# Kernel optimization log

Measured on AMD Instinct MI355X. Metric: run time of the kernel, lower is better.

The kernel has to match this reference:

```python
import jax, jax.numpy as jnp
import numpy as np

B, C, W, H = 32, 512, 28, 28  # input spatial = 2*init_width x 2*init_height
HEADS = 8


def setup_inputs() -> dict:
    key = jax.random.key(0)
    ks = jax.random.split(key, 9)
    d = C // HEADS
    s = 0.05
    return {
        "x": jax.random.normal(ks[0], (B, C, W, H), jnp.float32),
        # 1x1 conv weights == dense [out_c, in_c] + bias
        "wq": jax.random.normal(ks[1], (C, C), jnp.float32) * s,
        "bq": jax.random.normal(ks[2], (C,), jnp.float32) * s,
        "wk": jax.random.normal(ks[3], (C, C), jnp.float32) * s,
        "bk": jax.random.normal(ks[4], (C,), jnp.float32) * s,
        "wv": jax.random.normal(ks[5], (C, C), jnp.float32) * s,
        "bv": jax.random.normal(ks[6], (C,), jnp.float32) * s,
        "rel_h": jax.random.normal(ks[7], (1, HEADS, d, 1, H), jnp.float32),
        "rel_w": jax.random.normal(ks[8], (1, HEADS, d, W, 1), jnp.float32),
    }


def reference(x, wq, bq, wk, bk, wv, bv, rel_h, rel_w):
    b, c, w, h = x.shape
    heads = rel_h.shape[1]
    d = c // heads
    n = w * h

    def proj(wt, bi):
        # 1x1 conv == per-pixel dense over channels
        y = jnp.einsum('oc,bcwh->bowh', wt, x) + bi[None, :, None, None]
        return y.reshape(b, heads, d, n)  # [B, H, d, N]

    q = proj(wq, bq)
    k = proj(wk, bk)
    v = proj(wv, bv)

    # content-content: q^T k -> [B, H, N, N]
    cc = jnp.einsum('bhdn,bhdm->bhnm', q, k)
    # relative position bias: (rel_h + rel_w) broadcast to [H, d, 2w0*2h0] = [H, d, N]
    pos = (rel_h + rel_w).reshape(heads, d, n)
    # content-position: pos^T @ q -> [B, H, N, N]
    cp = jnp.einsum('hdp,bhdn->bhpn', pos, q)

    attn = jax.nn.softmax(cc + cp, axis=-1)  # softmax over last dim
    # out = v @ attn^T : [B, H, d, N]
    out = jnp.einsum('bhdn,bhmn->bhdm', v, attn)
    return out.reshape(b, c, w, h)
```

## Files before the change

### kernel.cpp

```cpp
#include <hip/hip_runtime.h>


#define BATCH 32
#define CCH   512
#define NHEAD 8
#define DH    64
#define NTOK  784
#define WSP   28
#define OT    128
#define NT    112
#define WLD   40
#define CH    64
#define NCHUNK 13
#define NIBLK  7
#define KQLD  136
#define VLD   72

typedef unsigned short u16;
typedef unsigned int   u32;
typedef short  short8  __attribute__((ext_vector_type(8)));
typedef float  floatx4 __attribute__((ext_vector_type(4)));

__device__ __forceinline__ u16 f2bf(float f) {
    union { float f; u32 i; } v; v.f = f;
    u32 x = v.i;
    return (u16)((x + 0x7FFFu + ((x >> 16) & 1u)) >> 16);
}
__device__ __forceinline__ u32 f2u(float f) { union { float f; u32 i; } v; v.f = f; return v.i; }
__device__ __forceinline__ float u2f(u32 u) { union { u32 i; float f; } v; v.i = u; return v.f; }

__device__ __forceinline__ u32 packsplit(float f) {
    const u32 hib = f2u(f) & 0xFFFF0000u;
    const float lo = f - u2f(hib);
    return ((u32)f2bf(lo) << 16) | (hib >> 16);
}

__global__ __launch_bounds__(256)
void pack_weights(const float* __restrict__ wq, const float* __restrict__ wk,
                  const float* __restrict__ wv,
                  u32* __restrict__ Wqp, u32* __restrict__ Wkp, u32* __restrict__ Wvp)
{
    const int i = blockIdx.x * 256 + threadIdx.x;
    if (i < CCH * CCH) {
        Wqp[i] = packsplit(wq[i]);
        Wkp[i] = packsplit(wk[i]);
        Wvp[i] = packsplit(wv[i]);
    }
}

__global__ __launch_bounds__(256)
void pack_x(const float* __restrict__ x, u32* __restrict__ Xp, int b0, size_t count)
{
    const size_t i = (size_t)blockIdx.x * 256 + threadIdx.x;
    if (i < count)
        Xp[i] = packsplit(x[(size_t)b0 * CCH * NTOK + i]);
}

__global__ __launch_bounds__(512)
void qkv_proj(const u32* __restrict__ Xp,
              const u32* __restrict__ Wqp, const float* __restrict__ bq,
              const u32* __restrict__ Wkp, const float* __restrict__ bk,
              const u32* __restrict__ Wvp, const float* __restrict__ bv,
              u32* __restrict__ Qp, u32* __restrict__ Kp, u16* __restrict__ Vo,
              int nbatch)
{
    const int t    = threadIdx.x;
    const int lane = t & 63;
    const int wid  = t >> 6;
    const int z    = blockIdx.z;
    const int proj = z / nbatch;
    const int bl   = z - proj * nbatch;
    const int o0   = blockIdx.y * OT;
    const int n0   = blockIdx.x * NT;

    const u32*   Wp   = (proj == 0) ? Wqp : (proj == 1) ? Wkp : Wvp;
    const float* bias = (proj == 0) ? bq  : (proj == 1) ? bk  : bv;

    __shared__ u16 wh[OT][WLD], wl[OT][WLD];
    __shared__ u16 xh[NT][WLD], xl[NT][WLD];

    const int m    = lane & 15;
    const int quad = lane >> 4;

    floatx4 acc[7];
    #pragma unroll
    for (int j = 0; j < 7; j++) acc[j] = (floatx4){0.f, 0.f, 0.f, 0.f};

    const int wo = t >> 2;
    const int wc = (t & 3) * 8;
    const int xc = t >> 3;
    const int xn = (t & 7) * 14;

    const size_t xbase = (size_t)bl * CCH * NTOK;

    for (int c0 = 0; c0 < CCH; c0 += 32) {
        uint4 wv0 = *reinterpret_cast<const uint4*>(&Wp[(size_t)(o0 + wo) * CCH + c0 + wc]);
        uint4 wv1 = *reinterpret_cast<const uint4*>(&Wp[(size_t)(o0 + wo) * CCH + c0 + wc + 4]);
        u32 xreg[14];
        if (t < 256) {
            #pragma unroll
            for (int u = 0; u < 7; u++) {
                const uint2 p = *reinterpret_cast<const uint2*>(&Xp[xbase + (size_t)(c0 + xc) * NTOK + n0 + xn + 2 * u]);
                xreg[2 * u] = p.x; xreg[2 * u + 1] = p.y;
            }
        }
        __syncthreads();
        {
            const u32 wr[8] = {wv0.x, wv0.y, wv0.z, wv0.w, wv1.x, wv1.y, wv1.z, wv1.w};
            ushort4 h0 = make_ushort4((u16)(wr[0] & 0xFFFF), (u16)(wr[1] & 0xFFFF), (u16)(wr[2] & 0xFFFF), (u16)(wr[3] & 0xFFFF));
            ushort4 h1 = make_ushort4((u16)(wr[4] & 0xFFFF), (u16)(wr[5] & 0xFFFF), (u16)(wr[6] & 0xFFFF), (u16)(wr[7] & 0xFFFF));
            ushort4 l0 = make_ushort4((u16)(wr[0] >> 16), (u16)(wr[1] >> 16), (u16)(wr[2] >> 16), (u16)(wr[3] >> 16));
            ushort4 l1 = make_ushort4((u16)(wr[4] >> 16), (u16)(wr[5] >> 16), (u16)(wr[6] >> 16), (u16)(wr[7] >> 16));
            *reinterpret_cast<ushort4*>(&wh[wo][wc])     = h0;
            *reinterpret_cast<ushort4*>(&wh[wo][wc + 4]) = h1;
            *reinterpret_cast<ushort4*>(&wl[wo][wc])     = l0;
            *reinterpret_cast<ushort4*>(&wl[wo][wc + 4]) = l1;
        }
        if (t < 256) {
            #pragma unroll
            for (int u = 0; u < 14; u++) {
                xh[xn + u][xc] = (u16)(xreg[u] & 0xFFFFu);
                xl[xn + u][xc] = (u16)(xreg[u] >> 16);
            }
        }
        __syncthreads();

        const short8 Ah = *reinterpret_cast<const short8*>(&wh[wid * 16 + m][quad * 8]);
        const short8 Al = *reinterpret_cast<const short8*>(&wl[wid * 16 + m][quad * 8]);
        #pragma unroll
        for (int jt = 0; jt < 7; jt++) {
            const short8 Bh = *reinterpret_cast<const short8*>(&xh[jt * 16 + m][quad * 8]);
            const short8 Bl = *reinterpret_cast<const short8*>(&xl[jt * 16 + m][quad * 8]);
            acc[jt] = __builtin_amdgcn_mfma_f32_16x16x32_bf16(Ah, Bh, acc[jt], 0, 0, 0);
            acc[jt] = __builtin_amdgcn_mfma_f32_16x16x32_bf16(Ah, Bl, acc[jt], 0, 0, 0);
            acc[jt] = __builtin_amdgcn_mfma_f32_16x16x32_bf16(Al, Bh, acc[jt], 0, 0, 0);
        }
    }

    const size_t obase = (size_t)bl * CCH * NTOK;
    #pragma unroll
    for (int r = 0; r < 4; r++) {
        const int o = o0 + wid * 16 + quad * 4 + r;
        const float bi = bias[o];
        #pragma unroll
        for (int jt = 0; jt < 7; jt++) {
            const int n = n0 + jt * 16 + m;
            const float val = acc[jt][r] + bi;
            const size_t idx = obase + (size_t)o * NTOK + n;
            if (proj == 0)      Qp[idx] = packsplit(val);
            else if (proj == 1) Kp[idx] = packsplit(val);
            else                Vo[idx] = f2bf(val);
        }
    }
}

__global__ __launch_bounds__(512)
void attn_kernel(const u32* __restrict__ Qp, const u32* __restrict__ Kp,
                 const u16* __restrict__ V,
                 const float* __restrict__ rel_h, const float* __restrict__ rel_w,
                 float* __restrict__ out, int b0)
{
    const int t    = threadIdx.x;
    const int lane = t & 63;
    const int wid  = t >> 6;
    const int m    = lane & 15;
    const int quad = lane >> 4;
    const int bl   = blockIdx.x;
    const int h    = blockIdx.y;
    int i0 = blockIdx.z * 128;
    if (i0 > NTOK - 128) i0 = NTOK - 128;
    const int b  = b0 + bl;
    const int hd = h * DH;
    const size_t base  = ((size_t)bl * CCH + hd) * NTOK;
    const size_t baseo = ((size_t)b  * CCH + hd) * NTOK;

    __shared__ u16 kqh[CH][KQLD];
    __shared__ u16 kql[CH][KQLD];
    __shared__ u16 vt[DH][VLD];
    __shared__ u16 pt[128][VLD];

    short8 Bh[4], Bl[4];
    {
        const int ig = i0 + wid * 16 + m;
        const int iw = ig / WSP, ih = ig % WSP;
        #pragma unroll
        for (int c = 0; c < 4; c++) {
            union { short8 v; u16 u[8]; } hb, lb;
            #pragma unroll
            for (int idx = 0; idx < 8; idx++) {
                const int k = c * 32 + quad * 8 + idx;
                if (k < DH) {
                    const u32 p = Qp[base + (size_t)k * NTOK + ig];
                    hb.u[idx] = (u16)(p & 0xFFFFu);
                    lb.u[idx] = (u16)(p >> 16);
                } else {
                    const int d = k - DH;
                    const float pos = rel_h[(size_t)(hd + d) * WSP + ih]
                                    + rel_w[(size_t)(hd + d) * WSP + iw];
                    const u32 hib = f2u(pos) & 0xFFFF0000u;
                    hb.u[idx] = (u16)(hib >> 16);
                    lb.u[idx] = f2bf(pos - u2f(hib));
                }
            }
            Bh[c] = hb.v; Bl[c] = lb.v;
        }
    }

    floatx4 Oacc[4];
    #pragma unroll
    for (int dt = 0; dt < 4; dt++) Oacc[dt] = (floatx4){0.f, 0.f, 0.f, 0.f};
    float mrun = -1e30f, lrun = 0.f;

    const int cg4 = (t & 31) * 4;
    const int jb4 = (t >> 5) * 4;
    const int vd  = t >> 3;
    const int vj  = (t & 7) * 8;

    for (int chn = 0; chn < NCHUNK; chn++) {
        const int j0 = chn * CH;
        __syncthreads();

        {
            u32 kv[4][4];
            #pragma unroll
            for (int cc = 0; cc < 4; cc++) {
                const int c = cg4 + cc;
                const u32* src = (c < DH) ? (Kp + base + (size_t)c * NTOK)
                                          : (Qp + base + (size_t)(c - DH) * NTOK);
                const uint4 a = *reinterpret_cast<const uint4*>(&src[j0 + jb4]);
                kv[cc][0] = a.x; kv[cc][1] = a.y; kv[cc][2] = a.z; kv[cc][3] = a.w;
            }
            #pragma unroll
            for (int jj = 0; jj < 4; jj++) {
                const ushort4 hi = make_ushort4((u16)(kv[0][jj] & 0xFFFFu), (u16)(kv[1][jj] & 0xFFFFu),
                                                (u16)(kv[2][jj] & 0xFFFFu), (u16)(kv[3][jj] & 0xFFFFu));
                const ushort4 lo = make_ushort4((u16)(kv[0][jj] >> 16), (u16)(kv[1][jj] >> 16),
                                                (u16)(kv[2][jj] >> 16), (u16)(kv[3][jj] >> 16));
                *reinterpret_cast<ushort4*>(&kqh[jb4 + jj][cg4]) = hi;
                *reinterpret_cast<ushort4*>(&kql[jb4 + jj][cg4]) = lo;
            }
        }
        if (j0 + vj + 8 <= NTOK) {
            const uint4 a = *reinterpret_cast<const uint4*>(&V[base + (size_t)vd * NTOK + j0 + vj]);
            *reinterpret_cast<uint4*>(&vt[vd][vj]) = a;
        } else {
            #pragma unroll
            for (int u = 0; u < 8; u++)
                vt[vd][vj + u] = (j0 + vj + u < NTOK) ? V[base + (size_t)vd * NTOK + j0 + vj + u] : (u16)0;
        }
        __syncthreads();

        floatx4 Sacc[4];
        #pragma unroll
        for (int js = 0; js < 4; js++) Sacc[js] = (floatx4){0.f, 0.f, 0.f, 0.f};
        #pragma unroll
        for (int c = 0; c < 4; c++) {
            #pragma unroll
            for (int js = 0; js < 4; js++) {
                const short8 Ah = *reinterpret_cast<const short8*>(&kqh[js * 16 + m][c * 32 + quad * 8]);
                const short8 Al = *reinterpret_cast<const short8*>(&kql[js * 16 + m][c * 32 + quad * 8]);
                Sacc[js] = __builtin_amdgcn_mfma_f32_16x16x32_bf16(Ah, Bh[c], Sacc[js], 0, 0, 0);
                Sacc[js] = __builtin_amdgcn_mfma_f32_16x16x32_bf16(Ah, Bl[c], Sacc[js], 0, 0, 0);
                Sacc[js] = __builtin_amdgcn_mfma_f32_16x16x32_bf16(Al, Bh[c], Sacc[js], 0, 0, 0);
            }
        }

        float sv[16];
        #pragma unroll
        for (int js = 0; js < 4; js++)
            #pragma unroll
            for (int r = 0; r < 4; r++) sv[js * 4 + r] = Sacc[js][r];
        if (j0 + CH > NTOK) {
            #pragma unroll
            for (int js = 0; js < 4; js++)
                #pragma unroll
                for (int r = 0; r < 4; r++)
                    if (j0 + js * 16 + quad * 4 + r >= NTOK) sv[js * 4 + r] = -1e30f;
        }
        float mc = sv[0];
        #pragma unroll
        for (int u = 1; u < 16; u++) mc = fmaxf(mc, sv[u]);
        mc = fmaxf(mc, __shfl_xor(mc, 16, 64));
        mc = fmaxf(mc, __shfl_xor(mc, 32, 64));
        const float mnew  = fmaxf(mrun, mc);
        const float alpha = __expf(mrun - mnew);
        float ps = 0.f;
        #pragma unroll
        for (int u = 0; u < 16; u++) {
            const float p = __expf(sv[u] - mnew);
            sv[u] = p;
            ps += p;
        }
        ps += __shfl_xor(ps, 16, 64);
        ps += __shfl_xor(ps, 32, 64);
        lrun = lrun * alpha + ps;
        mrun = mnew;
        #pragma unroll
        for (int dt = 0; dt < 4; dt++)
            #pragma unroll
            for (int r = 0; r < 4; r++) Oacc[dt][r] *= alpha;

        #pragma unroll
        for (int js = 0; js < 4; js++) {
            const ushort4 pw = make_ushort4(f2bf(sv[js * 4 + 0]), f2bf(sv[js * 4 + 1]),
                                            f2bf(sv[js * 4 + 2]), f2bf(sv[js * 4 + 3]));
            *reinterpret_cast<ushort4*>(&pt[wid * 16 + m][js * 16 + quad * 4]) = pw;
        }

        #pragma unroll
        for (int joff = 0; joff < CH; joff += 32) {
            const short8 Bp = *reinterpret_cast<const short8*>(&pt[wid * 16 + m][joff + quad * 8]);
            #pragma unroll
            for (int dt = 0; dt < 4; dt++) {
                const short8 Av = *reinterpret_cast<const short8*>(&vt[dt * 16 + m][joff + quad * 8]);
                Oacc[dt] = __builtin_amdgcn_mfma_f32_16x16x32_bf16(Av, Bp, Oacc[dt], 0, 0, 0);
            }
        }
    }

    const float linv = 1.f / lrun;
    #pragma unroll
    for (int dt = 0; dt < 4; dt++) {
        #pragma unroll
        for (int r = 0; r < 4; r++) {
            const int d = dt * 16 + quad * 4 + r;
            out[baseo + (size_t)d * NTOK + i0 + wid * 16 + m] = Oacc[dt][r] * linv;
        }
    }
}

extern "C" void kernel_launch(void* const* d_in, const int* in_sizes, int n_in,
                              void* d_out, int out_size, void* d_ws, size_t ws_size,
                              hipStream_t stream)
{
    const float* x  = (const float*)d_in[0];
    const float* wq = (const float*)d_in[1];
    const float* bq = (const float*)d_in[2];
    const float* wk = (const float*)d_in[3];
    const float* bk = (const float*)d_in[4];
    const float* wv = (const float*)d_in[5];
    const float* bv = (const float*)d_in[6];
    const float* rh = (const float*)d_in[7];
    const float* rw = (const float*)d_in[8];
    float* out = (float*)d_out;

    const size_t perB = (size_t)CCH * NTOK;
    const size_t WELEM = (size_t)CCH * CCH;
    const size_t weightBytes = 3 * WELEM * 4;
    const size_t perBatchBytes = perB * 14;

    size_t avail = (ws_size > weightBytes) ? (ws_size - weightBytes) : perBatchBytes;
    size_t nb_s = avail / perBatchBytes;
    int nb = (int)(nb_s < 1 ? 1 : (nb_s > BATCH ? BATCH : nb_s));

    u32* Wqp = (u32*)d_ws;
    u32* Wkp = Wqp + WELEM;
    u32* Wvp = Wkp + WELEM;
    u32* chunk0 = Wvp + WELEM;

    pack_weights<<<dim3((CCH * CCH + 255) / 256), dim3(256), 0, stream>>>(wq, wk, wv, Wqp, Wkp, Wvp);

    for (int b0 = 0; b0 < BATCH; b0 += nb) {
        const int curb = (BATCH - b0 < nb) ? (BATCH - b0) : nb;
        u32* Xp = chunk0;
        u32* Qp = Xp + (size_t)curb * perB;
        u32* Kp = Qp + (size_t)curb * perB;
        u16* Vb = (u16*)(Kp + (size_t)curb * perB);

        const size_t xcount = (size_t)curb * perB;
        pack_x<<<dim3((unsigned)((xcount + 255) / 256)), dim3(256), 0, stream>>>(x, Xp, b0, xcount);

        dim3 gp(NTOK / NT, CCH / OT, 3 * curb);
        qkv_proj<<<gp, dim3(512), 0, stream>>>(Xp, Wqp, bq, Wkp, bk, Wvp, bv,
                                               Qp, Kp, Vb, curb);

        dim3 ga(curb, NHEAD, NIBLK);
        attn_kernel<<<ga, dim3(512), 0, stream>>>(Qp, Kp, Vb, rh, rw, out, b0);
    }
}
```

Baseline: 526.2 us.

## Prefetch next K/Q/V chunk into registers during attention compute, raise MFMA priority

Moves the global loads of the next chunk's K/Q and V tiles into registers before the current chunk's MFMA work, so memory latency overlaps compute instead of stalling each iteration. The LDS stores from those registers happen at the top of the next iteration. It also wraps the MFMA sections in s_setprio to favor matrix instructions across waves. This costs extra registers for the prefetched data, which may lower occupancy.

```diff
diff --git a/kernel.cpp b/kernel.cpp
--- a/kernel.cpp
+++ b/kernel.cpp
@@ -216,43 +216,54 @@
     const int vd  = t >> 3;
     const int vj  = (t & 7) * 8;
 
+    u32 kv[4][4];
+    union { uint4 v; u16 u[8]; } vreg;
+
+#define PREFETCH_CHUNK(J0)                                                                       \
+    {                                                                                            \
+        _Pragma("unroll")                                                                        \
+        for (int cc = 0; cc < 4; cc++) {                                                         \
+            const int c = cg4 + cc;                                                              \
+            const u32* src = (c < DH) ? (Kp + base + (size_t)c * NTOK)                           \
+                                      : (Qp + base + (size_t)(c - DH) * NTOK);                   \
+            const uint4 a = *reinterpret_cast<const uint4*>(&src[(J0) + jb4]);                   \
+            kv[cc][0] = a.x; kv[cc][1] = a.y; kv[cc][2] = a.z; kv[cc][3] = a.w;                  \
+        }                                                                                        \
+        if ((J0) + vj + 8 <= NTOK) {                                                             \
+            vreg.v = *reinterpret_cast<const uint4*>(&V[base + (size_t)vd * NTOK + (J0) + vj]);  \
+        } else {                                                                                 \
+            _Pragma("unroll")                                                                    \
+            for (int u = 0; u < 8; u++)                                                          \
+                vreg.u[u] = ((J0) + vj + u < NTOK) ? V[base + (size_t)vd * NTOK + (J0) + vj + u] \
+                                                   : (u16)0;                                     \
+        }                                                                                        \
+    }
+
+    PREFETCH_CHUNK(0)
+
     for (int chn = 0; chn < NCHUNK; chn++) {
         const int j0 = chn * CH;
         __syncthreads();
 
-        {
-            u32 kv[4][4];
-            #pragma unroll
-            for (int cc = 0; cc < 4; cc++) {
-                const int c = cg4 + cc;
-                const u32* src = (c < DH) ? (Kp + base + (size_t)c * NTOK)
-                                          : (Qp + base + (size_t)(c - DH) * NTOK);
-                const uint4 a = *reinterpret_cast<const uint4*>(&src[j0 + jb4]);
-                kv[cc][0] = a.x; kv[cc][1] = a.y; kv[cc][2] = a.z; kv[cc][3] = a.w;
-            }
-            #pragma unroll
-            for (int jj = 0; jj < 4; jj++) {
-                const ushort4 hi = make_ushort4((u16)(kv[0][jj] & 0xFFFFu), (u16)(kv[1][jj] & 0xFFFFu),
-                                                (u16)(kv[2][jj] & 0xFFFFu), (u16)(kv[3][jj] & 0xFFFFu));
-                const ushort4 lo = make_ushort4((u16)(kv[0][jj] >> 16), (u16)(kv[1][jj] >> 16),
-                                                (u16)(kv[2][jj] >> 16), (u16)(kv[3][jj] >> 16));
-                *reinterpret_cast<ushort4*>(&kqh[jb4 + jj][cg4]) = hi;
-                *reinterpret_cast<ushort4*>(&kql[jb4 + jj][cg4]) = lo;
-            }
-        }
-        if (j0 + vj + 8 <= NTOK) {
-            const uint4 a = *reinterpret_cast<const uint4*>(&V[base + (size_t)vd * NTOK + j0 + vj]);
-            *reinterpret_cast<uint4*>(&vt[vd][vj]) = a;
-        } else {
-            #pragma unroll
-            for (int u = 0; u < 8; u++)
-                vt[vd][vj + u] = (j0 + vj + u < NTOK) ? V[base + (size_t)vd * NTOK + j0 + vj + u] : (u16)0;
-        }
+        #pragma unroll
+        for (int jj = 0; jj < 4; jj++) {
+            const ushort4 hi = make_ushort4((u16)(kv[0][jj] & 0xFFFFu), (u16)(kv[1][jj] & 0xFFFFu),
+                                            (u16)(kv[2][jj] & 0xFFFFu), (u16)(kv[3][jj] & 0xFFFFu));
+            const ushort4 lo = make_ushort4((u16)(kv[0][jj] >> 16), (u16)(kv[1][jj] >> 16),
+                                            (u16)(kv[2][jj] >> 16), (u16)(kv[3][jj] >> 16));
+            *reinterpret_cast<ushort4*>(&kqh[jb4 + jj][cg4]) = hi;
+            *reinterpret_cast<ushort4*>(&kql[jb4 + jj][cg4]) = lo;
+        }
+        *reinterpret_cast<uint4*>(&vt[vd][vj]) = vreg.v;
         __syncthreads();
 
+        if (chn + 1 < NCHUNK) PREFETCH_CHUNK(j0 + CH)
+        __builtin_amdgcn_sched_barrier(0);
+
         floatx4 Sacc[4];
         #pragma unroll
         for (int js = 0; js < 4; js++) Sacc[js] = (floatx4){0.f, 0.f, 0.f, 0.f};
+        __builtin_amdgcn_s_setprio(1);
         #pragma unroll
         for (int c = 0; c < 4; c++) {
             #pragma unroll
@@ -264,6 +275,7 @@
                 Sacc[js] = __builtin_amdgcn_mfma_f32_16x16x32_bf16(Al, Bh[c], Sacc[js], 0, 0, 0);
             }
         }
+        __builtin_amdgcn_s_setprio(0);
 
         float sv[16];
         #pragma unroll
@@ -307,6 +319,7 @@
             *reinterpret_cast<ushort4*>(&pt[wid * 16 + m][js * 16 + quad * 4]) = pw;
         }
 
+        __builtin_amdgcn_s_setprio(1);
         #pragma unroll
         for (int joff = 0; joff < CH; joff += 32) {
             const short8 Bp = *reinterpret_cast<const short8*>(&pt[wid * 16 + m][joff + quad * 8]);
@@ -316,7 +329,9 @@
                 Oacc[dt] = __builtin_amdgcn_mfma_f32_16x16x32_bf16(Av, Bp, Oacc[dt], 0, 0, 0);
             }
         }
-    }
+        __builtin_amdgcn_s_setprio(0);
+    }
+#undef PREFETCH_CHUNK
 
     const float linv = 1.f / lrun;
     #pragma unroll
```

Result: slower. 584.9 us (+11.1%).
